# Kernel optimization log

Measured on AMD Instinct MI355X. Metric: run time of the kernel, lower is better.

## Reference

```python
import jax, jax.numpy as jnp
import numpy as np

N = 1024        # batch of tokens (module is per-token; we vmap via batched einsums)
IN = 1024       # in_features
H = 16          # num_heads
D = 64          # head_dim
BD = 512        # binary_dim
M = 8192        # num memories
OUT = H * D     # out_features
TEMP = 0.01
EPS = 1e-5


def setup_inputs() -> dict:
    key = jax.random.key(0)
    ks = jax.random.split(key, 8)
    return {
        "x": jax.random.normal(ks[0], (N, IN), jnp.float32),
        "Wq": jax.random.normal(ks[1], (OUT, IN), jnp.float32) / np.sqrt(IN).astype(np.float32),
        "bq_bias": jax.random.normal(ks[2], (OUT,), jnp.float32) * 0.01,
        "bin_proj": jax.random.normal(ks[3], (H, BD, D), jnp.float32),
        "bin_inv": jax.random.normal(ks[4], (H, D, BD), jnp.float32) / np.float32(BD),
        # binary memory codes in {-1, +1}
        "weight_matrix": jnp.sign(jax.random.normal(ks[5], (H, M, BD), jnp.float32)),
        "ln_w": jnp.ones((OUT,), jnp.float32),
        "ln_b": jnp.zeros((OUT,), jnp.float32),
    }


def reference(x, Wq, bq_bias, bin_proj, bin_inv, weight_matrix, ln_w, ln_b):
    # query projection: [N, OUT] -> [N, H, D], L2-normalize per head
    q = (x @ Wq.T + bq_bias).reshape(N, H, D)
    q = q / jnp.linalg.norm(q, axis=-1, keepdims=True)
    # sign-encode into binary space: [N, H, BD]
    code = jnp.sign(jnp.einsum('nhd,hbd->nhb', q, bin_proj))
    # cosine-transformed Hamming-similarity scores: [N, H, M]
    sim = jnp.einsum('nhb,hmb->nhm', code, weight_matrix) / np.float32(BD)
    scores = jnp.cos((np.float32(np.pi) / 2) * (1.0 - sim))
    attn = jax.nn.softmax(scores / np.float32(TEMP), axis=-1)
    # readout from binary memories, project back to real space
    out = jnp.einsum('nhm,hmb->nhb', attn, weight_matrix)
    out = jnp.einsum('nhb,hdb->nhd', out, bin_inv)
    out = out / jnp.linalg.norm(out, axis=-1, keepdims=True)
    out = out.reshape(N, OUT)
    # LayerNorm over out_features
    mu = jnp.mean(out, axis=-1, keepdims=True)
    var = jnp.var(out, axis=-1, keepdims=True)
    return (out - mu) / jnp.sqrt(var + np.float32(EPS)) * ln_w + ln_b
```

## Files before the change

### kernel.cpp

```cpp
#include <hip/hip_runtime.h>
#include <hip/hip_fp16.h>

#define NTOK 1024
#define INF  1024
#define NH   16
#define DH   64
#define BDIM 512
#define NMEM 8192
#define OUTF 1024
#define NWRD 16

typedef _Float16 f16x8 __attribute__((ext_vector_type(8)));
typedef float    f32x4 __attribute__((ext_vector_type(4)));
typedef int      i32x4 __attribute__((ext_vector_type(4)));

#define GLOAD16(G, L) __builtin_amdgcn_global_load_lds( \
    (const __attribute__((address_space(1))) unsigned int*)(G), \
    (__attribute__((address_space(3))) unsigned int*)(L), 16, 0, 0)

__device__ inline float score2(float s) {
  return 144.2695040889f * __sinf(s * 0.0030679615757712823f);
}

__global__ __launch_bounds__(256) void k_qgemm(const float* __restrict__ x,
    const float* __restrict__ Wq, const float* __restrict__ bq, float* __restrict__ q) {
  __shared__ float As[64][17];
  __shared__ float Bs[64][17];
  const int tx = threadIdx.x & 15, ty = threadIdx.x >> 4;
  const int n0 = blockIdx.y * 64, o0 = blockIdx.x * 64;
  const int r = threadIdx.x >> 2, c4 = (threadIdx.x & 3) * 4;
  float acc[4][4] = {};
  for (int k0 = 0; k0 < INF; k0 += 16) {
    float4 av = *(const float4*)&x[(size_t)(n0 + r) * INF + k0 + c4];
    float4 bv = *(const float4*)&Wq[(size_t)(o0 + r) * INF + k0 + c4];
    __syncthreads();
    As[r][c4+0] = av.x; As[r][c4+1] = av.y; As[r][c4+2] = av.z; As[r][c4+3] = av.w;
    Bs[r][c4+0] = bv.x; Bs[r][c4+1] = bv.y; Bs[r][c4+2] = bv.z; Bs[r][c4+3] = bv.w;
    __syncthreads();
    #pragma unroll
    for (int kk = 0; kk < 16; ++kk) {
      float a[4], b[4];
      #pragma unroll
      for (int i = 0; i < 4; ++i) a[i] = As[ty*4+i][kk];
      #pragma unroll
      for (int j = 0; j < 4; ++j) b[j] = Bs[tx*4+j][kk];
      #pragma unroll
      for (int i = 0; i < 4; ++i)
        #pragma unroll
        for (int j = 0; j < 4; ++j) acc[i][j] += a[i] * b[j];
    }
  }
  #pragma unroll
  for (int i = 0; i < 4; ++i) {
    const int row = n0 + ty*4 + i;
    #pragma unroll
    for (int j = 0; j < 4; ++j) {
      const int col = o0 + tx*4 + j;
      q[(size_t)row * OUTF + col] = acc[i][j] + bq[col];
    }
  }
}

__global__ __launch_bounds__(256) void k_code(const float* __restrict__ q,
    const float* __restrict__ bp, signed char* __restrict__ code_i8) {
  const int h = blockIdx.y, n0 = blockIdx.x * 16;
  __shared__ float ql[16][68];
  const int t = threadIdx.x;
  {
    const int r = t >> 4, c = (t & 15) * 4;
    float4 v = *(const float4*)&q[(size_t)(n0 + r) * OUTF + h * 64 + c];
    ql[r][c] = v.x; ql[r][c+1] = v.y; ql[r][c+2] = v.z; ql[r][c+3] = v.w;
  }
  __syncthreads();
  #pragma unroll
  for (int bb = 0; bb < 512; bb += 256) {
    const int b = bb + t;
    float bpv[64];
    const float4* src = (const float4*)&bp[((size_t)h * BDIM + b) * 64];
    #pragma unroll
    for (int j = 0; j < 16; ++j) {
      float4 v = src[j];
      bpv[j*4] = v.x; bpv[j*4+1] = v.y; bpv[j*4+2] = v.z; bpv[j*4+3] = v.w;
    }
    for (int n = 0; n < 16; ++n) {
      float dot = 0.f;
      #pragma unroll
      for (int d = 0; d < 64; ++d) dot += bpv[d] * ql[n][d];
      code_i8[((size_t)h * NTOK + n0 + n) * BDIM + b] = dot > 0.f ? 1 : -1;
    }
  }
}

__global__ __launch_bounds__(256) void k_packw(const float* __restrict__ w,
    unsigned* __restrict__ wp, signed char* __restrict__ w_i8) {
  const int row  = blockIdx.x * 4 + (threadIdx.x >> 6);
  const int lane = threadIdx.x & 63;
  const float* src = w + (size_t)row * BDIM;
  unsigned my = 0;
  #pragma unroll
  for (int kk = 0; kk < 8; ++kk) {
    float v = src[kk * 64 + lane];
    w_i8[(size_t)row * BDIM + kk * 64 + lane] = v > 0.f ? 1 : -1;
    unsigned long long m = __ballot(v > 0.f);
    if ((lane >> 1) == kk) my = (lane & 1) ? (unsigned)(m >> 32) : (unsigned)m;
  }
  if (lane < 16) wp[(size_t)row * NWRD + lane] = my;
}

__global__ __launch_bounds__(256) void k_binT(const float* __restrict__ binv,
                                              float* __restrict__ bT) {
  const int h = blockIdx.y, b0 = blockIdx.x * 64;
  __shared__ float tl[64][65];
  const int t = threadIdx.x;
  #pragma unroll
  for (int i = 0; i < 4; ++i) {
    int fi = t + 256 * i;
    int d = fi >> 4, b = (fi & 15) * 4;
    float4 v = *(const float4*)&binv[((size_t)h * DH + d) * BDIM + b0 + b];
    tl[d][b] = v.x; tl[d][b+1] = v.y; tl[d][b+2] = v.z; tl[d][b+3] = v.w;
  }
  __syncthreads();
  #pragma unroll
  for (int i = 0; i < 4; ++i) {
    int fo = t + 256 * i;
    int bb = fo >> 4, dd = (fo & 15) * 4;
    float4 v = { tl[dd][bb], tl[dd+1][bb], tl[dd+2][bb], tl[dd+3][bb] };
    *(float4*)&bT[((size_t)h * BDIM + b0 + bb) * DH + dd] = v;
  }
}

__global__ __launch_bounds__(256) void k_wt(const unsigned* __restrict__ wp,
    unsigned short* __restrict__ wt, int h0) {
  const int hg = blockIdx.z, h = h0 + hg;
  const int b0 = blockIdx.y * 64, m0 = blockIdx.x * 256;
  __shared__ unsigned bits[256][2];
  const int t = threadIdx.x;
  const unsigned* src = wp + (size_t)(h * NMEM + m0 + t) * NWRD + (b0 >> 5);
  bits[t][0] = src[0]; bits[t][1] = src[1];
  __syncthreads();
  const int b = t >> 2, ms = (t & 3) * 64;
  const int wd = b >> 5, sh = b & 31;
  const int bx7 = b & 7;
  unsigned short* dst = wt + ((size_t)hg * BDIM + b0 + b) * NMEM + m0 + ms;
  #pragma unroll
  for (int g = 0; g < 8; ++g) {
    const int pg = g ^ bx7;
    const int j = ms + g * 8;
    ushort4 v0, v1;
    v0.x = ((bits[j+0][wd] >> sh) & 1) ? 0x3C00 : 0xBC00;
    v0.y = ((bits[j+1][wd] >> sh) & 1) ? 0x3C00 : 0xBC00;
    v0.z = ((bits[j+2][wd] >> sh) & 1) ? 0x3C00 : 0xBC00;
    v0.w = ((bits[j+3][wd] >> sh) & 1) ? 0x3C00 : 0xBC00;
    v1.x = ((bits[j+4][wd] >> sh) & 1) ? 0x3C00 : 0xBC00;
    v1.y = ((bits[j+5][wd] >> sh) & 1) ? 0x3C00 : 0xBC00;
    v1.z = ((bits[j+6][wd] >> sh) & 1) ? 0x3C00 : 0xBC00;
    v1.w = ((bits[j+7][wd] >> sh) & 1) ? 0x3C00 : 0xBC00;
    *(ushort4*)&dst[pg * 8]     = v0;
    *(ushort4*)&dst[pg * 8 + 4] = v1;
  }
}

__global__ __launch_bounds__(512, 2) void k_sim(const signed char* __restrict__ code_i8,
    const signed char* __restrict__ w_i8, short* __restrict__ simb,
    int h0, int gmask, int gshift) {
  const int bid = (int)blockIdx.x;
  const int hg = bid & gmask, h = h0 + hg;
  const int n0 = (bid >> gshift) * 64;
  const int t = threadIdx.x, lane = t & 63, wid = t >> 6;
  __shared__ int smaxl[64];
  __shared__ float sct[513];
  if (t < 64) smaxl[t] = -(1 << 30);
  for (int p = t; p < 513; p += 512)
    sct[p] = score2(2.f * (float)p - 512.f);
  i32x4 afrag[4][8];
  #pragma unroll
  for (int fi = 0; fi < 4; ++fi)
    #pragma unroll
    for (int kk = 0; kk < 8; ++kk)
      afrag[fi][kk] = *(const i32x4*)(code_i8 +
          ((size_t)h * NTOK + n0 + fi * 16 + (lane & 15)) * BDIM +
          kk * 64 + (lane >> 4) * 16);
  __syncthreads();
  int vmax[4][4];
  #pragma unroll
  for (int fi = 0; fi < 4; ++fi)
    #pragma unroll
    for (int j = 0; j < 4; ++j) vmax[fi][j] = -(1 << 30);
  const signed char* bbase0 = w_i8 + (size_t)h * NMEM * BDIM +
                              (lane & 15) * BDIM + (lane >> 4) * 16;
  short* srow = simb + ((size_t)hg * NTOK + n0) * NMEM;
  for (int i = 0; i < 32; ++i) {
    const int m0 = (i * 8 + wid) * 32;
    const signed char* bb = bbase0 + (size_t)m0 * BDIM;
    i32x4 acc[4][2] = {};
    #pragma unroll
    for (int kk = 0; kk < 8; ++kk) {
      i32x4 b0 = *(const i32x4*)(bb + kk * 64);
      i32x4 b1 = *(const i32x4*)(bb + 16 * BDIM + kk * 64);
      #pragma unroll
      for (int fi = 0; fi < 4; ++fi) {
        acc[fi][0] = __builtin_amdgcn_mfma_i32_16x16x64_i8(afrag[fi][kk], b0, acc[fi][0], 0, 0, 0);
        acc[fi][1] = __builtin_amdgcn_mfma_i32_16x16x64_i8(afrag[fi][kk], b1, acc[fi][1], 0, 0, 0);
      }
    }
    #pragma unroll
    for (int fi = 0; fi < 4; ++fi)
      #pragma unroll
      for (int j = 0; j < 4; ++j) {
        const int row = fi * 16 + (lane >> 4) * 4 + j;
        short* dst = srow + (size_t)row * NMEM + m0 + (lane & 15);
        const int v0 = acc[fi][0][j], v1 = acc[fi][1][j];
        dst[0]  = (short)v0;
        dst[16] = (short)v1;
        vmax[fi][j] = max(vmax[fi][j], max(v0, v1));
      }
  }
  #pragma unroll
  for (int fi = 0; fi < 4; ++fi)
    #pragma unroll
    for (int j = 0; j < 4; ++j) {
      int v = vmax[fi][j];
      #pragma unroll
      for (int s = 1; s < 16; s <<= 1) v = max(v, __shfl_xor(v, s));
      if ((lane & 15) == 0)
        atomicMax(&smaxl[fi * 16 + (lane >> 4) * 4 + j], v);
    }
  __syncthreads();
  unsigned short* arow = (unsigned short*)srow;
  for (int it = 0; it < 16; ++it) {
    const int gw = it * 512 + t;
    const int row = gw >> 7, win = gw & 127;
    const float sm2 = sct[(smaxl[row] + 512) >> 1];
    const short* sp = srow + (size_t)row * NMEM + win * 64;
    uint4 sv[8];
    #pragma unroll
    for (int c = 0; c < 8; ++c) sv[c] = *(const uint4*)(sp + c * 8);
    const int rx = row & 7;
    unsigned short* dp = arow + (size_t)row * NMEM + win * 64;
    #pragma unroll
    for (int c = 0; c < 8; ++c) {
      unsigned ov[4];
      #pragma unroll
      for (int k = 0; k < 4; ++k) {
        const unsigned w2 = (&sv[c].x)[k];
        const int lo = (int)(short)(w2 & 0xffffu);
        const int hi = (int)(short)(w2 >> 16);
        float p0 = exp2f(sct[(lo + 512) >> 1] - sm2);
        float p1 = exp2f(sct[(hi + 512) >> 1] - sm2);
        ov[k] = (unsigned)__half_as_ushort(__float2half(p0))
              | ((unsigned)__half_as_ushort(__float2half(p1)) << 16);
      }
      *(uint4*)(dp + (c ^ rx) * 8) = make_uint4(ov[0], ov[1], ov[2], ov[3]);
    }
  }
}

__global__ __launch_bounds__(512, 2) void k_stageF(const unsigned short* __restrict__ attn,
    const unsigned short* __restrict__ wt, float* __restrict__ o1t,
    int gmask, int gshift) {
  __shared__ _Float16 Al[128][64];
  __shared__ _Float16 Bl[128][64];
  const int wg = (int)blockIdx.x;
  const int hg = wg & gmask;
  const int rest = wg >> gshift;
  const int nt = rest & 7, bt = rest >> 3;
  const int n0 = nt * 128, b0 = bt * 128;
  const int t = threadIdx.x;
  const int lane = t & 63, wid = t >> 6;
  const int wm = wid >> 2, wn = wid & 3;
  f32x4 acc[4][2];
  #pragma unroll
  for (int i = 0; i < 4; ++i)
    #pragma unroll
    for (int j = 0; j < 2; ++j) acc[i][j] = (f32x4){0.f, 0.f, 0.f, 0.f};

  const unsigned short* ag = attn + ((size_t)hg * NTOK + n0 + 16*wid + (lane >> 3)) * NMEM + (lane & 7) * 8;
  const unsigned short* bg = wt   + ((size_t)hg * BDIM + b0 + 16*wid + (lane >> 3)) * NMEM + (lane & 7) * 8;
  _Float16* al0 = &Al[16 * wid][0];
  _Float16* bl0 = &Bl[16 * wid][0];

  for (int k0 = 0; k0 < NMEM; k0 += 64) {
    __syncthreads();
    GLOAD16(ag + k0,            al0);
    GLOAD16(ag + k0 + 8 * NMEM, al0 + 8 * 64);
    GLOAD16(bg + k0,            bl0);
    GLOAD16(bg + k0 + 8 * NMEM, bl0 + 8 * 64);
    __syncthreads();
    #pragma unroll
    for (int kk = 0; kk < 64; kk += 32) {
      const int phys = (((kk >> 3) + (lane >> 4)) ^ (lane & 7)) * 8;
      f16x8 af[4], bf[2];
      #pragma unroll
      for (int fm = 0; fm < 4; ++fm)
        af[fm] = *(const f16x8*)&Al[wm*64 + fm*16 + (lane & 15)][phys];
      #pragma unroll
      for (int fn = 0; fn < 2; ++fn)
        bf[fn] = *(const f16x8*)&Bl[wn*32 + fn*16 + (lane & 15)][phys];
      #pragma unroll
      for (int fm = 0; fm < 4; ++fm)
        #pragma unroll
        for (int fn = 0; fn < 2; ++fn)
          acc[fm][fn] = __builtin_amdgcn_mfma_f32_16x16x32_f16(af[fm], bf[fn], acc[fm][fn], 0, 0, 0);
    }
  }
  #pragma unroll
  for (int fm = 0; fm < 4; ++fm) {
    const int rowb = n0 + wm*64 + fm*16 + (lane >> 4) * 4;
    #pragma unroll
    for (int fn = 0; fn < 2; ++fn) {
      const int col = b0 + wn*32 + fn*16 + (lane & 15);
      *(f32x4*)&o1t[((size_t)hg * BDIM + col) * NTOK + rowb] = acc[fm][fn];
    }
  }
}

__global__ __launch_bounds__(256) void k_proj(const float* __restrict__ o1t,
    const float* __restrict__ bT, float* __restrict__ o2, int h0) {
  const int hg = blockIdx.y, h = h0 + hg;
  const int n0 = blockIdx.x * 64;
  __shared__ float bl[128][68];
  __shared__ float ol[128][68];
  __shared__ float outl[64][68];
  __shared__ float nrm[64];
  const int t = threadIdx.x;
  const int tx = t & 15, ty = t >> 4;
  float acc[4][4] = {};
  for (int c = 0; c < 4; ++c) {
    const int bb0 = c * 128;
    __syncthreads();
    #pragma unroll
    for (int i = 0; i < 8; ++i) {
      int fi = t + 256 * i;
      int rr = fi >> 4, cc = (fi & 15) * 4;
      *(float4*)&bl[rr][cc] = *(const float4*)&bT[((size_t)h * BDIM + bb0 + rr) * DH + cc];
      *(float4*)&ol[rr][cc] = *(const float4*)&o1t[((size_t)hg * BDIM + bb0 + rr) * NTOK + n0 + cc];
    }
    __syncthreads();
    for (int bb = 0; bb < 128; ++bb) {
      float4 bd = *(const float4*)&bl[bb][tx * 4];
      float4 on = *(const float4*)&ol[bb][ty * 4];
      float ai[4] = {on.x, on.y, on.z, on.w};
      float bj[4] = {bd.x, bd.y, bd.z, bd.w};
      #pragma unroll
      for (int i = 0; i < 4; ++i)
        #pragma unroll
        for (int j = 0; j < 4; ++j) acc[i][j] += ai[i] * bj[j];
    }
  }
  __syncthreads();
  #pragma unroll
  for (int i = 0; i < 4; ++i)
    #pragma unroll
    for (int j = 0; j < 4; ++j) outl[ty*4 + i][tx*4 + j] = acc[i][j];
  __syncthreads();
  if (t < 64) {
    float s = 0.f;
    #pragma unroll
    for (int d = 0; d < 64; ++d) { float v = outl[t][d]; s += v * v; }
    nrm[t] = 1.f / sqrtf(s);
  }
  __syncthreads();
  {
    const int n = t >> 2, dg = (t & 3) * 16;
    #pragma unroll
    for (int j = 0; j < 16; ++j)
      o2[(size_t)(n0 + n) * OUTF + h * 64 + dg + j] = outl[n][dg + j] * nrm[n];
  }
}

__global__ __launch_bounds__(256) void k_ln(const float* __restrict__ o2,
    const float* __restrict__ lnw, const float* __restrict__ lnb, float* __restrict__ out) {
  const int n = blockIdx.x, t = threadIdx.x;
  __shared__ float red[4];
  float4 v = *(const float4*)&o2[(size_t)n * OUTF + t * 4];
  float s = v.x + v.y + v.z + v.w;
  const int lane = t & 63, wid = t >> 6;
  #pragma unroll
  for (int off = 32; off; off >>= 1) s += __shfl_down(s, off);
  if (lane == 0) red[wid] = s;
  __syncthreads();
  const float mu = (red[0] + red[1] + red[2] + red[3]) * (1.f / 1024.f);
  float4 d = {v.x - mu, v.y - mu, v.z - mu, v.w - mu};
  float s2 = d.x*d.x + d.y*d.y + d.z*d.z + d.w*d.w;
  #pragma unroll
  for (int off = 32; off; off >>= 1) s2 += __shfl_down(s2, off);
  __syncthreads();
  if (lane == 0) red[wid] = s2;
  __syncthreads();
  const float var = (red[0] + red[1] + red[2] + red[3]) * (1.f / 1024.f);
  const float inv = 1.f / sqrtf(var + 1e-5f);
  float4 w = *(const float4*)&lnw[t * 4];
  float4 b = *(const float4*)&lnb[t * 4];
  float4 o = { d.x*inv*w.x + b.x, d.y*inv*w.y + b.y,
               d.z*inv*w.z + b.z, d.w*inv*w.w + b.w };
  *(float4*)&out[(size_t)n * OUTF + t * 4] = o;
}

extern "C" void kernel_launch(void* const* d_in, const int* in_sizes, int n_in,
                              void* d_out, int out_size, void* d_ws, size_t ws_size,
                              hipStream_t stream) {
  (void)in_sizes; (void)n_in; (void)out_size;
  const float* x    = (const float*)d_in[0];
  const float* Wq   = (const float*)d_in[1];
  const float* bq   = (const float*)d_in[2];
  const float* bp   = (const float*)d_in[3];
  const float* binv = (const float*)d_in[4];
  const float* wm   = (const float*)d_in[5];
  const float* lnw  = (const float*)d_in[6];
  const float* lnb  = (const float*)d_in[7];
  float* outp = (float*)d_out;

  char* ws = (char*)d_ws;
  size_t off = 0;
  auto carve = [&](size_t bytes) -> char* {
    char* p = ws + off;
    off += (bytes + 255) & ~(size_t)255;
    return p;
  };
  float*       q       = (float*)      carve((size_t)NTOK * OUTF * 4);
  signed char* code_i8 = (signed char*)carve((size_t)NH * NTOK * BDIM);
  unsigned*    wpk     = (unsigned*)   carve((size_t)NH * NMEM * NWRD * 4);
  signed char* w_i8    = (signed char*)carve((size_t)NH * NMEM * BDIM);
  float*       bT      = (float*)      carve((size_t)NH * BDIM * DH * 4);
  float*       o2      = (float*)      carve((size_t)NTOK * OUTF * 4);
  const size_t fixed = off;
  const size_t per = ((size_t)BDIM * NMEM * 2 + 256)
                   + ((size_t)NTOK * NMEM * 2 + 256)
                   + ((size_t)BDIM * NTOK * 4 + 256);
  int G = 16;
  while (G > 1 && fixed + (size_t)G * per > ws_size) G >>= 1;
  unsigned short* wt   = (unsigned short*)carve((size_t)G * BDIM * NMEM * 2);
  short*          simb = (short*)         carve((size_t)G * NTOK * NMEM * 2);
  float*          o1t  = (float*)         carve((size_t)G * BDIM * NTOK * 4);
  const int gshift = __builtin_ctz(G);

  k_qgemm<<<dim3(16, 16), 256, 0, stream>>>(x, Wq, bq, q);
  k_code <<<dim3(64, 16), 256, 0, stream>>>(q, bp, code_i8);
  k_packw<<<dim3(NH * NMEM / 4), 256, 0, stream>>>(wm, wpk, w_i8);
  k_binT <<<dim3(8, 16), 256, 0, stream>>>(binv, bT);
  for (int h0 = 0; h0 < NH; h0 += G) {
    k_wt    <<<dim3(32, 8, G), 256, 0, stream>>>(wpk, wt, h0);
    k_sim   <<<dim3(16 * G),   512, 0, stream>>>(code_i8, w_i8, simb, h0, G - 1, gshift);
    k_stageF<<<dim3(32 * G),   512, 0, stream>>>((const unsigned short*)simb, wt, o1t, G - 1, gshift);
    k_proj  <<<dim3(16, G),    256, 0, stream>>>(o1t, bT, o2, h0);
  }
  k_ln<<<dim3(NTOK), 256, 0, stream>>>(o2, lnw, lnb, outp);
}
```

Measured before the change: 783.3 us.

## Recompute similarity GEMM twice in k_sim instead of storing and rereading int16 scores

k_sim now makes two passes of the int8 MFMA similarity GEMM. The first pass only finds each row's maximum; the second recomputes the GEMM and writes the fp16 softmax numerators directly. This removes the int16 sim write plus the full reread and rewrite of the NTOK×NMEM buffer. It also switches to 32x32x32 MFMA tiles with the code tile staged in swizzled LDS, runs 768 threads with 12 waves, and drops the score lookup table in favour of computing the sine directly. The cost is twice the MFMA work and twice the weight reads, plus scattered 2-byte global stores.

```diff
diff --git a/kernel.cpp b/kernel.cpp
--- a/kernel.cpp
+++ b/kernel.cpp
@@ -13,6 +13,7 @@
 typedef _Float16 f16x8 __attribute__((ext_vector_type(8)));
 typedef float    f32x4 __attribute__((ext_vector_type(4)));
 typedef int      i32x4 __attribute__((ext_vector_type(4)));
+typedef int      i32x16 __attribute__((ext_vector_type(16)));
 
 #define GLOAD16(G, L) __builtin_amdgcn_global_load_lds( \
     (const __attribute__((address_space(1))) unsigned int*)(G), \
@@ -160,98 +161,112 @@
   }
 }
 
-__global__ __launch_bounds__(512, 2) void k_sim(const signed char* __restrict__ code_i8,
-    const signed char* __restrict__ w_i8, short* __restrict__ simb,
+__global__ __launch_bounds__(768, 1) void k_sim(const signed char* __restrict__ code_i8,
+    const signed char* __restrict__ w_i8, unsigned short* __restrict__ attn,
     int h0, int gmask, int gshift) {
   const int bid = (int)blockIdx.x;
   const int hg = bid & gmask, h = h0 + hg;
   const int n0 = (bid >> gshift) * 64;
   const int t = threadIdx.x, lane = t & 63, wid = t >> 6;
+  __shared__ signed char Als[64 * 512];
   __shared__ int smaxl[64];
-  __shared__ float sct[513];
   if (t < 64) smaxl[t] = -(1 << 30);
-  for (int p = t; p < 513; p += 512)
-    sct[p] = score2(2.f * (float)p - 512.f);
-  i32x4 afrag[4][8];
-  #pragma unroll
-  for (int fi = 0; fi < 4; ++fi)
-    #pragma unroll
-    for (int kk = 0; kk < 8; ++kk)
-      afrag[fi][kk] = *(const i32x4*)(code_i8 +
-          ((size_t)h * NTOK + n0 + fi * 16 + (lane & 15)) * BDIM +
-          kk * 64 + (lane >> 4) * 16);
-  __syncthreads();
-  int vmax[4][4];
-  #pragma unroll
-  for (int fi = 0; fi < 4; ++fi)
-    #pragma unroll
-    for (int j = 0; j < 4; ++j) vmax[fi][j] = -(1 << 30);
-  const signed char* bbase0 = w_i8 + (size_t)h * NMEM * BDIM +
-                              (lane & 15) * BDIM + (lane >> 4) * 16;
-  short* srow = simb + ((size_t)hg * NTOK + n0) * NMEM;
-  for (int i = 0; i < 32; ++i) {
-    const int m0 = (i * 8 + wid) * 32;
-    const signed char* bb = bbase0 + (size_t)m0 * BDIM;
-    i32x4 acc[4][2] = {};
-    #pragma unroll
-    for (int kk = 0; kk < 8; ++kk) {
-      i32x4 b0 = *(const i32x4*)(bb + kk * 64);
-      i32x4 b1 = *(const i32x4*)(bb + 16 * BDIM + kk * 64);
-      #pragma unroll
-      for (int fi = 0; fi < 4; ++fi) {
-        acc[fi][0] = __builtin_amdgcn_mfma_i32_16x16x64_i8(afrag[fi][kk], b0, acc[fi][0], 0, 0, 0);
-        acc[fi][1] = __builtin_amdgcn_mfma_i32_16x16x64_i8(afrag[fi][kk], b1, acc[fi][1], 0, 0, 0);
+  if (t < 512) {
+    const int row = t >> 3;
+    const signed char* src = code_i8 + ((size_t)h * NTOK + n0 + row) * BDIM + (t & 7) * 64;
+    const int rx = row & 7;
+    #pragma unroll
+    for (int u = 0; u < 4; ++u) {
+      const int c = (t & 7) * 4 + u;
+      const int p = (c & ~7) | ((c & 7) ^ rx);
+      *(i32x4*)&Als[row * 512 + p * 16] = *(const i32x4*)(src + u * 16);
+    }
+  }
+  __syncthreads();
+  const int l31 = lane & 31, l5 = lane >> 5, l7 = lane & 7;
+  const signed char* bbase = w_i8 + (size_t)h * NMEM * BDIM +
+                             (size_t)l31 * BDIM + l5 * 16;
+  int vmax[2][16];
+  #pragma unroll
+  for (int fi = 0; fi < 2; ++fi)
+    #pragma unroll
+    for (int r = 0; r < 16; ++r) vmax[fi][r] = -(1 << 30);
+  for (int i = wid; i < 128; i += 12) {
+    const int m0 = i * 64;
+    unsigned ab = 0;
+    asm volatile("" : "+v"(ab));
+    const signed char* bb = bbase + (size_t)m0 * BDIM;
+    i32x16 acc[2][2] = {};
+    #pragma unroll 4
+    for (int kk = 0; kk < 16; ++kk) {
+      i32x4 b0 = *(const i32x4*)(bb + kk * 32);
+      i32x4 b1 = *(const i32x4*)(bb + 32 * BDIM + kk * 32);
+      const int c = kk * 2 + l5;
+      const unsigned p = (unsigned)((c & ~7) | ((c & 7) ^ l7)) * 16u;
+      i32x4 a0 = *(const i32x4*)&Als[ab + (unsigned)l31 * 512u + p];
+      i32x4 a1 = *(const i32x4*)&Als[ab + (unsigned)(l31 + 32) * 512u + p];
+      acc[0][0] = __builtin_amdgcn_mfma_i32_32x32x32_i8(a0, b0, acc[0][0], 0, 0, 0);
+      acc[1][0] = __builtin_amdgcn_mfma_i32_32x32x32_i8(a1, b0, acc[1][0], 0, 0, 0);
+      acc[0][1] = __builtin_amdgcn_mfma_i32_32x32x32_i8(a0, b1, acc[0][1], 0, 0, 0);
+      acc[1][1] = __builtin_amdgcn_mfma_i32_32x32x32_i8(a1, b1, acc[1][1], 0, 0, 0);
+    }
+    #pragma unroll
+    for (int fi = 0; fi < 2; ++fi)
+      #pragma unroll
+      for (int r = 0; r < 16; ++r)
+        vmax[fi][r] = max(vmax[fi][r], max(acc[fi][0][r], acc[fi][1][r]));
+  }
+  #pragma unroll
+  for (int fi = 0; fi < 2; ++fi)
+    #pragma unroll
+    for (int r = 0; r < 16; ++r) {
+      int v = vmax[fi][r];
+      #pragma unroll
+      for (int s = 1; s < 32; s <<= 1) v = max(v, __shfl_xor(v, s));
+      if (l31 == 0)
+        atomicMax(&smaxl[fi * 32 + (r & 3) + 8 * (r >> 2) + 4 * l5], v);
+    }
+  __syncthreads();
+  float sm2[2][16];
+  #pragma unroll
+  for (int fi = 0; fi < 2; ++fi)
+    #pragma unroll
+    for (int r = 0; r < 16; ++r)
+      sm2[fi][r] = score2((float)smaxl[fi * 32 + (r & 3) + 8 * (r >> 2) + 4 * l5]);
+  for (int i = wid; i < 128; i += 12) {
+    const int m0 = i * 64;
+    unsigned ab = 0;
+    asm volatile("" : "+v"(ab));
+    const signed char* bb = bbase + (size_t)m0 * BDIM;
+    i32x16 acc[2][2] = {};
+    #pragma unroll 4
+    for (int kk = 0; kk < 16; ++kk) {
+      i32x4 b0 = *(const i32x4*)(bb + kk * 32);
+      i32x4 b1 = *(const i32x4*)(bb + 32 * BDIM + kk * 32);
+      const int c = kk * 2 + l5;
+      const unsigned p = (unsigned)((c & ~7) | ((c & 7) ^ l7)) * 16u;
+      i32x4 a0 = *(const i32x4*)&Als[ab + (unsigned)l31 * 512u + p];
+      i32x4 a1 = *(const i32x4*)&Als[ab + (unsigned)(l31 + 32) * 512u + p];
+      acc[0][0] = __builtin_amdgcn_mfma_i32_32x32x32_i8(a0, b0, acc[0][0], 0, 0, 0);
+      acc[1][0] = __builtin_amdgcn_mfma_i32_32x32x32_i8(a1, b0, acc[1][0], 0, 0, 0);
+      acc[0][1] = __builtin_amdgcn_mfma_i32_32x32x32_i8(a0, b1, acc[0][1], 0, 0, 0);
+      acc[1][1] = __builtin_amdgcn_mfma_i32_32x32x32_i8(a1, b1, acc[1][1], 0, 0, 0);
+    }
+    #pragma unroll
+    for (int fi = 0; fi < 2; ++fi)
+      #pragma unroll
+      for (int r = 0; r < 16; ++r) {
+        const int row = n0 + fi * 32 + (r & 3) + 8 * (r >> 2) + 4 * l5;
+        const int r7 = (r & 3) | (l5 << 2);
+        unsigned short* dro = attn + ((size_t)hg * NTOK + row) * NMEM;
+        #pragma unroll
+        for (int mj = 0; mj < 2; ++mj) {
+          const int m = m0 + mj * 32 + l31;
+          const int ms = (m & ~63) | ((((m >> 3) & 7) ^ r7) << 3) | (m & 7);
+          float pr = exp2f(score2((float)acc[fi][mj][r]) - sm2[fi][r]);
+          dro[ms] = __half_as_ushort(__float2half(pr));
+        }
       }
-    }
-    #pragma unroll
-    for (int fi = 0; fi < 4; ++fi)
-      #pragma unroll
-      for (int j = 0; j < 4; ++j) {
-        const int row = fi * 16 + (lane >> 4) * 4 + j;
-        short* dst = srow + (size_t)row * NMEM + m0 + (lane & 15);
-        const int v0 = acc[fi][0][j], v1 = acc[fi][1][j];
-        dst[0]  = (short)v0;
-        dst[16] = (short)v1;
-        vmax[fi][j] = max(vmax[fi][j], max(v0, v1));
-      }
-  }
-  #pragma unroll
-  for (int fi = 0; fi < 4; ++fi)
-    #pragma unroll
-    for (int j = 0; j < 4; ++j) {
-      int v = vmax[fi][j];
-      #pragma unroll
-      for (int s = 1; s < 16; s <<= 1) v = max(v, __shfl_xor(v, s));
-      if ((lane & 15) == 0)
-        atomicMax(&smaxl[fi * 16 + (lane >> 4) * 4 + j], v);
-    }
-  __syncthreads();
-  unsigned short* arow = (unsigned short*)srow;
-  for (int it = 0; it < 16; ++it) {
-    const int gw = it * 512 + t;
-    const int row = gw >> 7, win = gw & 127;
-    const float sm2 = sct[(smaxl[row] + 512) >> 1];
-    const short* sp = srow + (size_t)row * NMEM + win * 64;
-    uint4 sv[8];
-    #pragma unroll
-    for (int c = 0; c < 8; ++c) sv[c] = *(const uint4*)(sp + c * 8);
-    const int rx = row & 7;
-    unsigned short* dp = arow + (size_t)row * NMEM + win * 64;
-    #pragma unroll
-    for (int c = 0; c < 8; ++c) {
-      unsigned ov[4];
-      #pragma unroll
-      for (int k = 0; k < 4; ++k) {
-        const unsigned w2 = (&sv[c].x)[k];
-        const int lo = (int)(short)(w2 & 0xffffu);
-        const int hi = (int)(short)(w2 >> 16);
-        float p0 = exp2f(sct[(lo + 512) >> 1] - sm2);
-        float p1 = exp2f(sct[(hi + 512) >> 1] - sm2);
-        ov[k] = (unsigned)__half_as_ushort(__float2half(p0))
-              | ((unsigned)__half_as_ushort(__float2half(p1)) << 16);
-      }
-      *(uint4*)(dp + (c ^ rx) * 8) = make_uint4(ov[0], ov[1], ov[2], ov[3]);
-    }
   }
 }
 
@@ -430,7 +445,7 @@
   int G = 16;
   while (G > 1 && fixed + (size_t)G * per > ws_size) G >>= 1;
   unsigned short* wt   = (unsigned short*)carve((size_t)G * BDIM * NMEM * 2);
-  short*          simb = (short*)         carve((size_t)G * NTOK * NMEM * 2);
+  unsigned short* attn = (unsigned short*)carve((size_t)G * NTOK * NMEM * 2);
   float*          o1t  = (float*)         carve((size_t)G * BDIM * NTOK * 4);
   const int gshift = __builtin_ctz(G);
 
@@ -440,8 +455,8 @@
   k_binT <<<dim3(8, 16), 256, 0, stream>>>(binv, bT);
   for (int h0 = 0; h0 < NH; h0 += G) {
     k_wt    <<<dim3(32, 8, G), 256, 0, stream>>>(wpk, wt, h0);
-    k_sim   <<<dim3(16 * G),   512, 0, stream>>>(code_i8, w_i8, simb, h0, G - 1, gshift);
-    k_stageF<<<dim3(32 * G),   512, 0, stream>>>((const unsigned short*)simb, wt, o1t, G - 1, gshift);
+    k_sim   <<<dim3(16 * G),   768, 0, stream>>>(code_i8, w_i8, attn, h0, G - 1, gshift);
+    k_stageF<<<dim3(32 * G),   512, 0, stream>>>(attn, wt, o1t, G - 1, gshift);
     k_proj  <<<dim3(16, G),    256, 0, stream>>>(o1t, bT, o2, h0);
   }
   k_ln<<<dim3(NTOK), 256, 0, stream>>>(o2, lnw, lnb, outp);
```

New measurement: 851.9 us. +8.8%, slower.

## Shrink k_sim token tile to 16 rows with 256-thread blocks for more parallelism

Applied to the files above, without the earlier changes.

Each k_sim block now handles 16 tokens instead of 64, with 4 waves of 256 threads and 4x as many blocks. Each wave computes a single 16x16 MFMA tile per iteration instead of 4x2 tiles. This cuts register pressure and raises occupancy and block count. In exchange, every memory-code fragment loaded from global memory is reused across 16 tokens instead of 64, so reads of w_i8 grow about fourfold.

```diff
diff --git a/kernel.cpp b/kernel.cpp
--- a/kernel.cpp
+++ b/kernel.cpp
@@ -160,75 +160,56 @@
   }
 }
 
-__global__ __launch_bounds__(512, 2) void k_sim(const signed char* __restrict__ code_i8,
+__global__ __launch_bounds__(256, 4) void k_sim(const signed char* __restrict__ code_i8,
     const signed char* __restrict__ w_i8, short* __restrict__ simb,
     int h0, int gmask, int gshift) {
   const int bid = (int)blockIdx.x;
   const int hg = bid & gmask, h = h0 + hg;
-  const int n0 = (bid >> gshift) * 64;
+  const int n0 = (bid >> gshift) * 16;
   const int t = threadIdx.x, lane = t & 63, wid = t >> 6;
-  __shared__ int smaxl[64];
+  __shared__ int smaxl[16];
   __shared__ float sct[513];
-  if (t < 64) smaxl[t] = -(1 << 30);
-  for (int p = t; p < 513; p += 512)
+  if (t < 16) smaxl[t] = -(1 << 30);
+  for (int p = t; p < 513; p += 256)
     sct[p] = score2(2.f * (float)p - 512.f);
-  i32x4 afrag[4][8];
-  #pragma unroll
-  for (int fi = 0; fi < 4; ++fi)
-    #pragma unroll
-    for (int kk = 0; kk < 8; ++kk)
-      afrag[fi][kk] = *(const i32x4*)(code_i8 +
-          ((size_t)h * NTOK + n0 + fi * 16 + (lane & 15)) * BDIM +
-          kk * 64 + (lane >> 4) * 16);
-  __syncthreads();
-  int vmax[4][4];
-  #pragma unroll
-  for (int fi = 0; fi < 4; ++fi)
-    #pragma unroll
-    for (int j = 0; j < 4; ++j) vmax[fi][j] = -(1 << 30);
-  const signed char* bbase0 = w_i8 + (size_t)h * NMEM * BDIM +
-                              (lane & 15) * BDIM + (lane >> 4) * 16;
+  i32x4 afrag[8];
+  #pragma unroll
+  for (int kk = 0; kk < 8; ++kk)
+    afrag[kk] = *(const i32x4*)(code_i8 +
+        ((size_t)h * NTOK + n0 + (lane & 15)) * BDIM + kk * 64 + (lane >> 4) * 16);
+  __syncthreads();
+  int vmax[4] = {-(1 << 30), -(1 << 30), -(1 << 30), -(1 << 30)};
+  const signed char* bbase = w_i8 + (size_t)h * NMEM * BDIM +
+                             (size_t)(lane & 15) * BDIM + (lane >> 4) * 16;
   short* srow = simb + ((size_t)hg * NTOK + n0) * NMEM;
-  for (int i = 0; i < 32; ++i) {
-    const int m0 = (i * 8 + wid) * 32;
-    const signed char* bb = bbase0 + (size_t)m0 * BDIM;
-    i32x4 acc[4][2] = {};
+  for (int i = 0; i < 128; ++i) {
+    const int m0 = (i * 4 + wid) * 16;
+    const signed char* bb = bbase + (size_t)m0 * BDIM;
+    i32x4 acc = {};
     #pragma unroll
     for (int kk = 0; kk < 8; ++kk) {
       i32x4 b0 = *(const i32x4*)(bb + kk * 64);
-      i32x4 b1 = *(const i32x4*)(bb + 16 * BDIM + kk * 64);
-      #pragma unroll
-      for (int fi = 0; fi < 4; ++fi) {
-        acc[fi][0] = __builtin_amdgcn_mfma_i32_16x16x64_i8(afrag[fi][kk], b0, acc[fi][0], 0, 0, 0);
-        acc[fi][1] = __builtin_amdgcn_mfma_i32_16x16x64_i8(afrag[fi][kk], b1, acc[fi][1], 0, 0, 0);
-      }
-    }
-    #pragma unroll
-    for (int fi = 0; fi < 4; ++fi)
-      #pragma unroll
-      for (int j = 0; j < 4; ++j) {
-        const int row = fi * 16 + (lane >> 4) * 4 + j;
-        short* dst = srow + (size_t)row * NMEM + m0 + (lane & 15);
-        const int v0 = acc[fi][0][j], v1 = acc[fi][1][j];
-        dst[0]  = (short)v0;
-        dst[16] = (short)v1;
-        vmax[fi][j] = max(vmax[fi][j], max(v0, v1));
-      }
-  }
-  #pragma unroll
-  for (int fi = 0; fi < 4; ++fi)
+      acc = __builtin_amdgcn_mfma_i32_16x16x64_i8(afrag[kk], b0, acc, 0, 0, 0);
+    }
     #pragma unroll
     for (int j = 0; j < 4; ++j) {
-      int v = vmax[fi][j];
-      #pragma unroll
-      for (int s = 1; s < 16; s <<= 1) v = max(v, __shfl_xor(v, s));
-      if ((lane & 15) == 0)
-        atomicMax(&smaxl[fi * 16 + (lane >> 4) * 4 + j], v);
-    }
+      const int row = (lane >> 4) * 4 + j;
+      srow[(size_t)row * NMEM + m0 + (lane & 15)] = (short)acc[j];
+      vmax[j] = max(vmax[j], acc[j]);
+    }
+  }
+  #pragma unroll
+  for (int j = 0; j < 4; ++j) {
+    int v = vmax[j];
+    #pragma unroll
+    for (int s = 1; s < 16; s <<= 1) v = max(v, __shfl_xor(v, s));
+    if ((lane & 15) == 0)
+      atomicMax(&smaxl[(lane >> 4) * 4 + j], v);
+  }
   __syncthreads();
   unsigned short* arow = (unsigned short*)srow;
-  for (int it = 0; it < 16; ++it) {
-    const int gw = it * 512 + t;
+  for (int it = 0; it < 8; ++it) {
+    const int gw = it * 256 + t;
     const int row = gw >> 7, win = gw & 127;
     const float sm2 = sct[(smaxl[row] + 512) >> 1];
     const short* sp = srow + (size_t)row * NMEM + win * 64;
@@ -440,7 +421,7 @@
   k_binT <<<dim3(8, 16), 256, 0, stream>>>(binv, bT);
   for (int h0 = 0; h0 < NH; h0 += G) {
     k_wt    <<<dim3(32, 8, G), 256, 0, stream>>>(wpk, wt, h0);
-    k_sim   <<<dim3(16 * G),   512, 0, stream>>>(code_i8, w_i8, simb, h0, G - 1, gshift);
+    k_sim   <<<dim3(64 * G),   256, 0, stream>>>(code_i8, w_i8, simb, h0, G - 1, gshift);
     k_stageF<<<dim3(32 * G),   512, 0, stream>>>((const unsigned short*)simb, wt, o1t, G - 1, gshift);
     k_proj  <<<dim3(16, G),    256, 0, stream>>>(o1t, bT, o2, h0);
   }
```

After: 1.021 ms. 30.4% more time.

## Stage swizzled int8 memory tiles in LDS for the sim kernel via direct global-to-LDS loads

Applied to the files above, without the earlier changes.

The int8 memory-code packing now writes each row with an XOR swizzle of its 16-byte chunks. k_sim stages 64-row tiles of those codes into a 32KB shared buffer using global_load_lds, so one copy is shared by all waves. Previously every wave loaded its B fragments straight from global memory. The wave layout changes to a 2x4 split (row group by memory group), which halves the per-wave A-fragment registers. In exchange there are two barriers per tile with no double-buffering, extra LDS use that may lower occupancy, and smaller MFMA work per wave.

```diff
diff --git a/kernel.cpp b/kernel.cpp
--- a/kernel.cpp
+++ b/kernel.cpp
@@ -100,7 +100,9 @@
   #pragma unroll
   for (int kk = 0; kk < 8; ++kk) {
     float v = src[kk * 64 + lane];
-    w_i8[(size_t)row * BDIM + kk * 64 + lane] = v > 0.f ? 1 : -1;
+    const int c = kk * 4 + (lane >> 4);
+    const int p = (c & ~7) | ((c & 7) ^ (row & 7));
+    w_i8[(size_t)row * BDIM + p * 16 + (lane & 15)] = v > 0.f ? 1 : -1;
     unsigned long long m = __ballot(v > 0.f);
     if ((lane >> 1) == kk) my = (lane & 1) ? (unsigned)(m >> 32) : (unsigned)m;
   }
@@ -167,63 +169,64 @@
   const int hg = bid & gmask, h = h0 + hg;
   const int n0 = (bid >> gshift) * 64;
   const int t = threadIdx.x, lane = t & 63, wid = t >> 6;
+  __shared__ __align__(16) signed char Bls[64 * 512];
+  __shared__ float sct[513];
   __shared__ int smaxl[64];
-  __shared__ float sct[513];
   if (t < 64) smaxl[t] = -(1 << 30);
   for (int p = t; p < 513; p += 512)
     sct[p] = score2(2.f * (float)p - 512.f);
-  i32x4 afrag[4][8];
-  #pragma unroll
-  for (int fi = 0; fi < 4; ++fi)
+  const int rg = wid >> 2, mg = wid & 3;
+  i32x4 afrag[2][8];
+  #pragma unroll
+  for (int fi = 0; fi < 2; ++fi)
     #pragma unroll
     for (int kk = 0; kk < 8; ++kk)
       afrag[fi][kk] = *(const i32x4*)(code_i8 +
-          ((size_t)h * NTOK + n0 + fi * 16 + (lane & 15)) * BDIM +
+          ((size_t)h * NTOK + n0 + rg * 32 + fi * 16 + (lane & 15)) * BDIM +
           kk * 64 + (lane >> 4) * 16);
-  __syncthreads();
-  int vmax[4][4];
-  #pragma unroll
-  for (int fi = 0; fi < 4; ++fi)
+  const signed char* wb = w_i8 + (size_t)h * NMEM * BDIM + (size_t)t * 16;
+  signed char* const d0 = &Bls[wid * 1024];
+  int vmax[2][4];
+  #pragma unroll
+  for (int fi = 0; fi < 2; ++fi)
     #pragma unroll
     for (int j = 0; j < 4; ++j) vmax[fi][j] = -(1 << 30);
-  const signed char* bbase0 = w_i8 + (size_t)h * NMEM * BDIM +
-                              (lane & 15) * BDIM + (lane >> 4) * 16;
   short* srow = simb + ((size_t)hg * NTOK + n0) * NMEM;
-  for (int i = 0; i < 32; ++i) {
-    const int m0 = (i * 8 + wid) * 32;
-    const signed char* bb = bbase0 + (size_t)m0 * BDIM;
-    i32x4 acc[4][2] = {};
+  for (int tile = 0; tile < 128; ++tile) {
+    const signed char* s = wb + (size_t)tile * 64 * BDIM;
+    __syncthreads();
+    GLOAD16(s, d0); GLOAD16(s + 8192, d0 + 8192);
+    GLOAD16(s + 16384, d0 + 16384); GLOAD16(s + 24576, d0 + 24576);
+    __syncthreads();
+    const signed char* bls = &Bls[(mg * 16 + (lane & 15)) * 512];
+    i32x4 acc0 = {}, acc1 = {};
     #pragma unroll
     for (int kk = 0; kk < 8; ++kk) {
-      i32x4 b0 = *(const i32x4*)(bb + kk * 64);
-      i32x4 b1 = *(const i32x4*)(bb + 16 * BDIM + kk * 64);
-      #pragma unroll
-      for (int fi = 0; fi < 4; ++fi) {
-        acc[fi][0] = __builtin_amdgcn_mfma_i32_16x16x64_i8(afrag[fi][kk], b0, acc[fi][0], 0, 0, 0);
-        acc[fi][1] = __builtin_amdgcn_mfma_i32_16x16x64_i8(afrag[fi][kk], b1, acc[fi][1], 0, 0, 0);
-      }
-    }
-    #pragma unroll
-    for (int fi = 0; fi < 4; ++fi)
-      #pragma unroll
-      for (int j = 0; j < 4; ++j) {
-        const int row = fi * 16 + (lane >> 4) * 4 + j;
-        short* dst = srow + (size_t)row * NMEM + m0 + (lane & 15);
-        const int v0 = acc[fi][0][j], v1 = acc[fi][1][j];
-        dst[0]  = (short)v0;
-        dst[16] = (short)v1;
-        vmax[fi][j] = max(vmax[fi][j], max(v0, v1));
-      }
-  }
-  #pragma unroll
-  for (int fi = 0; fi < 4; ++fi)
+      const int c = kk * 4 + (lane >> 4);
+      const int p = (c & ~7) | ((c & 7) ^ (lane & 7));
+      i32x4 b = *(const i32x4*)(bls + p * 16);
+      acc0 = __builtin_amdgcn_mfma_i32_16x16x64_i8(afrag[0][kk], b, acc0, 0, 0, 0);
+      acc1 = __builtin_amdgcn_mfma_i32_16x16x64_i8(afrag[1][kk], b, acc1, 0, 0, 0);
+    }
+    const int m0 = tile * 64 + mg * 16 + (lane & 15);
+    #pragma unroll
+    for (int j = 0; j < 4; ++j) {
+      const int r0 = rg * 32 + (lane >> 4) * 4 + j;
+      srow[(size_t)r0 * NMEM + m0]        = (short)acc0[j];
+      srow[(size_t)(r0 + 16) * NMEM + m0] = (short)acc1[j];
+      vmax[0][j] = max(vmax[0][j], acc0[j]);
+      vmax[1][j] = max(vmax[1][j], acc1[j]);
+    }
+  }
+  #pragma unroll
+  for (int fi = 0; fi < 2; ++fi)
     #pragma unroll
     for (int j = 0; j < 4; ++j) {
       int v = vmax[fi][j];
       #pragma unroll
       for (int s = 1; s < 16; s <<= 1) v = max(v, __shfl_xor(v, s));
       if ((lane & 15) == 0)
-        atomicMax(&smaxl[fi * 16 + (lane >> 4) * 4 + j], v);
+        atomicMax(&smaxl[rg * 32 + fi * 16 + (lane >> 4) * 4 + j], v);
     }
   __syncthreads();
   unsigned short* arow = (unsigned short*)srow;
@@ -258,8 +261,8 @@
 __global__ __launch_bounds__(512, 2) void k_stageF(const unsigned short* __restrict__ attn,
     const unsigned short* __restrict__ wt, float* __restrict__ o1t,
     int gmask, int gshift) {
-  __shared__ _Float16 Al[128][64];
-  __shared__ _Float16 Bl[128][64];
+  __shared__ __align__(16) _Float16 Al[128][64];
+  __shared__ __align__(16) _Float16 Bl[128][64];
   const int wg = (int)blockIdx.x;
   const int hg = wg & gmask;
   const int rest = wg >> gshift;
```

Measured after the change: 783.8 us. No clear change (+0.1%).
